# Optimization experiments

Hardware: AMD Instinct MI355X
Metric: run time of the kernel (lower is better)

## Reference

```python
import jax, jax.numpy as jnp
import numpy as np

N_NODES = 50000
N_EDGES = 800000
H = 128   # atom_hidden_feats
B = 64    # bond_in_feats
NEG_SLOPE = 0.01  # torch LeakyReLU default


def setup_inputs() -> dict:
    key = jax.random.key(0)
    k1, k2, k3, k4, k5 = jax.random.split(key, 5)
    feat = jax.random.normal(k1, (N_NODES, H), dtype=jnp.float32)
    gdf_feat = jax.random.normal(k2, (N_EDGES, B), dtype=jnp.float32)
    # Linear(2H+B -> H): weight [H, 2H+B], bias [H]
    W = jax.random.normal(k3, (H, 2 * H + B), dtype=jnp.float32) * 0.05
    b = jnp.zeros((H,), dtype=jnp.float32)
    src = jax.random.randint(k4, (N_EDGES,), 0, N_NODES, dtype=jnp.int64)
    dst = jax.random.randint(k5, (N_EDGES,), 0, N_NODES, dtype=jnp.int64)
    return {"feat": feat, "gdf_feat": gdf_feat, "W": W, "b": b, "src": src, "dst": dst}


def reference(feat, gdf_feat, W, b, src, dst):
    n_nodes = feat.shape[0]
    # Per-edge message: concat(src_feat, dst_feat, edge_feat) -> linear -> gate
    z = jnp.concatenate([feat[src], feat[dst], gdf_feat], axis=-1)  # [E, 2H+B]
    z = z @ W.T + b                                                 # [E, H]
    msg = jax.nn.sigmoid(z) * jnp.where(z > 0, z, NEG_SLOPE * z)    # sigmoid * leaky_relu
    # Scatter-sum messages to destination nodes
    return jax.ops.segment_sum(msg, dst, num_segments=n_nodes)      # [N, H]
```

## Files before the change

kernel.cpp:

```cpp
#include <hip/hip_runtime.h>
#include <hip/hip_bf16.h>

typedef __attribute__((ext_vector_type(8)))  short bf16x8;
typedef __attribute__((ext_vector_type(16))) float f32x16;
typedef __attribute__((ext_vector_type(4)))  float f32x4;

#define NN 50000
#define EE 800000
#define HH 128
#define KK 320
#define NEG 0.01f

__device__ __forceinline__ unsigned pack2(float a, float b) {
    unsigned short lo = __builtin_bit_cast(unsigned short, __float2bfloat16(a));
    unsigned short hi = __builtin_bit_cast(unsigned short, __float2bfloat16(b));
    return (unsigned)lo | ((unsigned)hi << 16);
}

__global__ __launch_bounds__(256, 2) void fused_edge_kernel(
    const float* __restrict__ feat, const float* __restrict__ gdf,
    const float* __restrict__ W,    const float* __restrict__ bias,
    const int*   __restrict__ src,  const int*   __restrict__ dst,
    float* __restrict__ out)
{
    __shared__ int4 lds4[64 * 40];
    __shared__ int  dsts[64];
    char* lds = (char*)lds4;

    const int tid  = threadIdx.x;
    const int lane = tid & 63;
    const int wid  = tid >> 6;
    const long long ebase = (long long)blockIdx.x * 64;

    const int col   = wid * 32 + (lane & 31);
    const int khalf = lane >> 5;
    bf16x8 Wb[20];
    {
        const float* wrow = W + col * KK + khalf * 8;
        #pragma unroll
        for (int k = 0; k < 20; k++) {
            f32x4 x0 = *(const f32x4*)(wrow + k * 16);
            f32x4 x1 = *(const f32x4*)(wrow + k * 16 + 4);
            union { bf16x8 v; unsigned u[4]; } t;
            t.u[0] = pack2(x0[0], x0[1]); t.u[1] = pack2(x0[2], x0[3]);
            t.u[2] = pack2(x1[0], x1[1]); t.u[3] = pack2(x1[2], x1[3]);
            Wb[k] = t.v;
        }
    }

    {
        const int r = tid >> 2, q = tid & 3;
        const long long e = ebase + r;
        const int s = src[e], d = dst[e];
        if (q == 0) dsts[r] = d;
        const float* fs = feat + (long long)s * HH;
        const float* fd = feat + (long long)d * HH;
        const float* ge = gdf  + (long long)e * 64;
        #pragma unroll
        for (int i = 0; i < 10; i++) {
            const int c = q + i * 4;
            const float* p = (c < 16) ? (fs + c * 8)
                           : (c < 32) ? (fd + (c - 16) * 8)
                                      : (ge + (c - 32) * 8);
            f32x4 v0 = *(const f32x4*)p;
            f32x4 v1 = *(const f32x4*)(p + 4);
            int4 h;
            h.x = (int)pack2(v0[0], v0[1]); h.y = (int)pack2(v0[2], v0[3]);
            h.z = (int)pack2(v1[0], v1[1]); h.w = (int)pack2(v1[2], v1[3]);
            *(int4*)(lds + r * 640 + ((c * 16) ^ ((r & 7) << 4))) = h;
        }
    }
    __syncthreads();

    f32x16 acc0 = {}; f32x16 acc1 = {};
    const int arow = lane & 31;
    const int xr   = (arow & 7) << 4;
    #pragma unroll
    for (int k = 0; k < 20; k++) {
        const int kb = k * 32 + khalf * 16;
        bf16x8 a0 = *(const bf16x8*)(lds + arow * 640 + (kb ^ xr));
        bf16x8 a1 = *(const bf16x8*)(lds + (arow + 32) * 640 + (kb ^ xr));
        acc0 = __builtin_amdgcn_mfma_f32_32x32x16_bf16(a0, Wb[k], acc0, 0, 0, 0);
        acc1 = __builtin_amdgcn_mfma_f32_32x32x16_bf16(a1, Wb[k], acc1, 0, 0, 0);
    }

    const float bv = bias[col];
    #pragma unroll
    for (int rt = 0; rt < 2; rt++) {
        const f32x16 A = rt ? acc1 : acc0;
        #pragma unroll
        for (int g = 0; g < 4; g++) {
            #pragma unroll
            for (int j = 0; j < 4; j++) {
                const int reg = g * 4 + j;
                const int row = j + g * 8 + khalf * 4;
                const float z  = A[reg] + bv;
                const float lr = z > 0.f ? z : NEG * z;
                const float sg = __builtin_amdgcn_rcpf(1.f + __expf(-z));
                const int dn = dsts[rt * 32 + row];
                unsafeAtomicAdd(out + (long long)dn * HH + col, lr * sg);
            }
        }
    }
}

extern "C" void kernel_launch(void* const* d_in, const int* in_sizes, int n_in,
                              void* d_out, int out_size, void* d_ws, size_t ws_size,
                              hipStream_t stream) {
    const float* feat = (const float*)d_in[0];
    const float* gdf  = (const float*)d_in[1];
    const float* W    = (const float*)d_in[2];
    const float* bias = (const float*)d_in[3];
    const int*   src  = (const int*)d_in[4];
    const int*   dst  = (const int*)d_in[5];
    float* out = (float*)d_out;

    hipMemsetAsync(out, 0, (size_t)out_size * sizeof(float), stream);
    fused_edge_kernel<<<EE / 64, 256, 0, stream>>>(feat, gdf, W, bias, src, dst, out);
}
```

Before: 377.9 us.

## Accumulate messages with packed fp16 atomics in a persistent edge-tile loop

Turns the kernel into a persistent loop over 768 blocks that prefetches the next tile's src/dst indices and raises occupancy to 3 blocks per SM. When workspace is large enough, adjacent output columns are packed into fp16 pairs via shuffle and added with global_atomic_pk_add_f16 into a half-precision accumulator, which a separate kernel then converts to fp32. This halves the number of atomic operations and the atomic traffic. The cost is fp16 accumulation precision, which may go past tolerance for nodes with many incoming edges, plus an extra conversion pass.

```diff
diff --git a/kernel.cpp b/kernel.cpp
--- a/kernel.cpp
+++ b/kernel.cpp
@@ -4,12 +4,15 @@
 typedef __attribute__((ext_vector_type(8)))  short bf16x8;
 typedef __attribute__((ext_vector_type(16))) float f32x16;
 typedef __attribute__((ext_vector_type(4)))  float f32x4;
+typedef __attribute__((ext_vector_type(2)))  __fp16 fp16x2;
 
 #define NN 50000
 #define EE 800000
 #define HH 128
 #define KK 320
 #define NEG 0.01f
+#define NTILES (EE / 64)
+#define NBLK 768
 
 __device__ __forceinline__ unsigned pack2(float a, float b) {
     unsigned short lo = __builtin_bit_cast(unsigned short, __float2bfloat16(a));
@@ -17,11 +20,12 @@
     return (unsigned)lo | ((unsigned)hi << 16);
 }
 
-__global__ __launch_bounds__(256, 2) void fused_edge_kernel(
+template<int USE_F16>
+__global__ __launch_bounds__(256, 3) void fused_edge_kernel(
     const float* __restrict__ feat, const float* __restrict__ gdf,
     const float* __restrict__ W,    const float* __restrict__ bias,
     const int*   __restrict__ src,  const int*   __restrict__ dst,
-    float* __restrict__ out)
+    float* __restrict__ out, __fp16* __restrict__ acc16)
 {
     __shared__ int4 lds4[64 * 40];
     __shared__ int  dsts[64];
@@ -30,10 +34,10 @@
     const int tid  = threadIdx.x;
     const int lane = tid & 63;
     const int wid  = tid >> 6;
-    const long long ebase = (long long)blockIdx.x * 64;
+    const int col  = wid * 32 + (lane & 31);
+    const int khalf = lane >> 5;
+    const int r = tid >> 2, q = tid & 3;
 
-    const int col   = wid * 32 + (lane & 31);
-    const int khalf = lane >> 5;
     bf16x8 Wb[20];
     {
         const float* wrow = W + col * KK + khalf * 8;
@@ -47,61 +51,98 @@
             Wb[k] = t.v;
         }
     }
+    const float bv = bias[col];
 
-    {
-        const int r = tid >> 2, q = tid & 3;
-        const long long e = ebase + r;
-        const int s = src[e], d = dst[e];
-        if (q == 0) dsts[r] = d;
-        const float* fs = feat + (long long)s * HH;
-        const float* fd = feat + (long long)d * HH;
-        const float* ge = gdf  + (long long)e * 64;
-        #pragma unroll
-        for (int i = 0; i < 10; i++) {
-            const int c = q + i * 4;
-            const float* p = (c < 16) ? (fs + c * 8)
-                           : (c < 32) ? (fd + (c - 16) * 8)
-                                      : (ge + (c - 32) * 8);
-            f32x4 v0 = *(const f32x4*)p;
-            f32x4 v1 = *(const f32x4*)(p + 4);
-            int4 h;
-            h.x = (int)pack2(v0[0], v0[1]); h.y = (int)pack2(v0[2], v0[3]);
-            h.z = (int)pack2(v1[0], v1[1]); h.w = (int)pack2(v1[2], v1[3]);
-            *(int4*)(lds + r * 640 + ((c * 16) ^ ((r & 7) << 4))) = h;
-        }
-    }
-    __syncthreads();
+    int tile = blockIdx.x;
+    int sCur = src[(long long)tile * 64 + r];
+    int dCur = dst[(long long)tile * 64 + r];
 
-    f32x16 acc0 = {}; f32x16 acc1 = {};
-    const int arow = lane & 31;
-    const int xr   = (arow & 7) << 4;
-    #pragma unroll
-    for (int k = 0; k < 20; k++) {
-        const int kb = k * 32 + khalf * 16;
-        bf16x8 a0 = *(const bf16x8*)(lds + arow * 640 + (kb ^ xr));
-        bf16x8 a1 = *(const bf16x8*)(lds + (arow + 32) * 640 + (kb ^ xr));
-        acc0 = __builtin_amdgcn_mfma_f32_32x32x16_bf16(a0, Wb[k], acc0, 0, 0, 0);
-        acc1 = __builtin_amdgcn_mfma_f32_32x32x16_bf16(a1, Wb[k], acc1, 0, 0, 0);
-    }
+    while (tile < NTILES) {
+        const long long ebase = (long long)tile * 64;
 
-    const float bv = bias[col];
-    #pragma unroll
-    for (int rt = 0; rt < 2; rt++) {
-        const f32x16 A = rt ? acc1 : acc0;
-        #pragma unroll
-        for (int g = 0; g < 4; g++) {
+        if (q == 0) dsts[r] = dCur;
+        {
+            const float* fs = feat + (long long)sCur * HH;
+            const float* fd = feat + (long long)dCur * HH;
+            const float* ge = gdf  + (ebase + r) * 64;
             #pragma unroll
-            for (int j = 0; j < 4; j++) {
-                const int reg = g * 4 + j;
-                const int row = j + g * 8 + khalf * 4;
-                const float z  = A[reg] + bv;
-                const float lr = z > 0.f ? z : NEG * z;
-                const float sg = __builtin_amdgcn_rcpf(1.f + __expf(-z));
-                const int dn = dsts[rt * 32 + row];
-                unsafeAtomicAdd(out + (long long)dn * HH + col, lr * sg);
+            for (int i = 0; i < 10; i++) {
+                const int c = q + i * 4;
+                const float* p = (c < 16) ? (fs + c * 8)
+                               : (c < 32) ? (fd + (c - 16) * 8)
+                                          : (ge + (c - 32) * 8);
+                f32x4 v0 = *(const f32x4*)p;
+                f32x4 v1 = *(const f32x4*)(p + 4);
+                int4 h;
+                h.x = (int)pack2(v0[0], v0[1]); h.y = (int)pack2(v0[2], v0[3]);
+                h.z = (int)pack2(v1[0], v1[1]); h.w = (int)pack2(v1[2], v1[3]);
+                *(int4*)(lds + r * 640 + ((c * 16) ^ ((r & 7) << 4))) = h;
             }
         }
+        __syncthreads();
+
+        const int nt = tile + NBLK;
+        if (nt < NTILES) {
+            sCur = src[(long long)nt * 64 + r];
+            dCur = dst[(long long)nt * 64 + r];
+        }
+
+        f32x16 acc0 = {}; f32x16 acc1 = {};
+        const int arow = lane & 31;
+        const int xr   = (arow & 7) << 4;
+        #pragma unroll
+        for (int k = 0; k < 20; k++) {
+            const int kb = k * 32 + khalf * 16;
+            bf16x8 a0 = *(const bf16x8*)(lds + arow * 640 + (kb ^ xr));
+            bf16x8 a1 = *(const bf16x8*)(lds + (arow + 32) * 640 + (kb ^ xr));
+            acc0 = __builtin_amdgcn_mfma_f32_32x32x16_bf16(a0, Wb[k], acc0, 0, 0, 0);
+            acc1 = __builtin_amdgcn_mfma_f32_32x32x16_bf16(a1, Wb[k], acc1, 0, 0, 0);
+        }
+
+        #pragma unroll
+        for (int rt = 0; rt < 2; rt++) {
+            const f32x16 A = rt ? acc1 : acc0;
+            #pragma unroll
+            for (int g = 0; g < 4; g++) {
+                #pragma unroll
+                for (int j = 0; j < 4; j++) {
+                    const int reg = g * 4 + j;
+                    const int row = j + g * 8 + khalf * 4;
+                    const float z  = A[reg] + bv;
+                    const float lr = z > 0.f ? z : NEG * z;
+                    const float sg = 1.f / (1.f + __expf(-z));
+                    const float m  = lr * sg;
+                    const int dn = dsts[rt * 32 + row];
+                    if (USE_F16) {
+                        const float o = __shfl_xor(m, 1);
+                        if (!(lane & 1)) {
+                            fp16x2 hv = __builtin_amdgcn_cvt_pkrtz(m, o);
+                            __fp16* p = acc16 + (long long)dn * HH + col;
+                            asm volatile("global_atomic_pk_add_f16 %0, %1, off"
+                                         :: "v"(p), "v"(hv) : "memory");
+                        }
+                    } else {
+                        unsafeAtomicAdd(out + (long long)dn * HH + col, m);
+                    }
+                }
+            }
+        }
+        __syncthreads();
+        tile = nt;
     }
+}
+
+__global__ __launch_bounds__(256) void conv_kernel(const int4* __restrict__ acc,
+                                                   float4* __restrict__ out)
+{
+    const int i = blockIdx.x * 256 + threadIdx.x;
+    union { int4 v; __fp16 h[8]; } u;
+    u.v = acc[i];
+    float4 a, b;
+    a.x = (float)u.h[0]; a.y = (float)u.h[1]; a.z = (float)u.h[2]; a.w = (float)u.h[3];
+    b.x = (float)u.h[4]; b.y = (float)u.h[5]; b.z = (float)u.h[6]; b.w = (float)u.h[7];
+    out[2 * i]     = a;
+    out[2 * i + 1] = b;
 }
 
 extern "C" void kernel_launch(void* const* d_in, const int* in_sizes, int n_in,
@@ -115,6 +156,16 @@
     const int*   dst  = (const int*)d_in[5];
     float* out = (float*)d_out;
 
-    hipMemsetAsync(out, 0, (size_t)out_size * sizeof(float), stream);
-    fused_edge_kernel<<<EE / 64, 256, 0, stream>>>(feat, gdf, W, bias, src, dst, out);
+    const size_t accBytes = (size_t)NN * HH * sizeof(__fp16);
+    if (ws_size >= accBytes) {
+        (void)hipMemsetAsync(d_ws, 0, accBytes, stream);
+        fused_edge_kernel<1><<<NBLK, 256, 0, stream>>>(feat, gdf, W, bias, src, dst,
+                                                       out, (__fp16*)d_ws);
+        conv_kernel<<<(NN * HH / 8) / 256, 256, 0, stream>>>((const int4*)d_ws,
+                                                             (float4*)out);
+    } else {
+        (void)hipMemsetAsync(out, 0, (size_t)out_size * sizeof(float), stream);
+        fused_edge_kernel<0><<<NBLK, 256, 0, stream>>>(feat, gdf, W, bias, src, dst,
+                                                       out, (__fp16*)d_ws);
+    }
 }
```

Measured after the change: 326.0 us. 13.7% less time.
